# Performance work log

Hardware: AMD Instinct MI355X
Metric: run time of the kernel (lower is better)

Reference implementation:

```python
import jax, jax.numpy as jnp
import numpy as np

T, B = 512, 64
D = [2048, 128]; P = [512, 128]; H = [256, 128]
A, S, OUT = 128, 128, 256
SC = 0.05


def setup_inputs() -> dict:
    key = jax.random.key(0)
    ks = iter(jax.random.split(key, 64))
    def n(shape, sc=SC):
        return jax.random.normal(next(ks), shape, dtype=jnp.float32) * sc
    inp = {
        "x0": n((T, B, D[0]), 1.0),
        "x1": n((T, B, D[1]), 1.0),
        "s": n((B, S), 1.0),
    }
    for m in range(2):
        k = str(m)
        C = 2 * H[m]
        inp["emb_w" + k] = n((D[m], P[m])); inp["emb_b" + k] = n((P[m],))
        inp["fx_w" + k] = n((P[m], 4 * H[m])); inp["fx_b" + k] = n((4 * H[m],))
        inp["fh_w" + k] = n((H[m], 4 * H[m]))
        inp["bx_w" + k] = n((P[m], 4 * H[m])); inp["bx_b" + k] = n((4 * H[m],))
        inp["bh_w" + k] = n((H[m], 4 * H[m]))
        inp["atV_w" + k] = n((C, A)); inp["atV_b" + k] = n((A,))
        inp["atW_w" + k] = n((S, A)); inp["atW_b" + k] = n((A,))
        inp["atw_w" + k] = n((A, 1)); inp["atw_b" + k] = n((1,))
        inp["lgd_w" + k] = n((C, OUT)); inp["lgd_b" + k] = n((OUT,))
    return inp


def _lstm_scan(xg, Wh, reverse=False):
    # xg: [T,B,4H] precomputed input projections; Wh: [H,4H]
    Tn, Bn, H4 = xg.shape
    Hn = H4 // 4
    def step(carry, xt):
        c, h = carry
        g = xt + h @ Wh
        a, i, f, o = jnp.split(g, 4, axis=-1)  # chunk order as in torch.split
        c = jnp.tanh(a) * jax.nn.sigmoid(i) + c * jax.nn.sigmoid(f)
        h = jnp.tanh(c) * jax.nn.sigmoid(o)
        return (c, h), h
    init = (jnp.zeros((Bn, Hn), xg.dtype), jnp.zeros((Bn, Hn), xg.dtype))
    _, hs = jax.lax.scan(step, init, xg, reverse=reverse)
    return hs  # [T,B,H]


def _encode_mod(x, emb_w, emb_b, fx_w, fx_b, fh_w, bx_w, bx_b, bh_w):
    h0 = x @ emb_w + emb_b                       # [T,B,P]
    hf = _lstm_scan(h0 @ fx_w + fx_b, fh_w)      # forward LSTM
    hb = _lstm_scan(h0 @ bx_w + bx_b, bh_w, reverse=True)  # backward LSTM
    return jnp.concatenate([hf, hb], axis=-1)    # [T,B,2H]


def _attend(h, s, atV_w, atV_b, atW_w, atW_b, atw_w, atw_b):
    vh = h @ atV_w + atV_b                       # [T,B,A]
    ws = s @ atW_w + atW_b                       # [B,A]
    logits = (jnp.tanh(vh + ws) @ atw_w)[..., 0] + atw_b[0]  # [T,B]
    a = jax.nn.softmax(logits, axis=0)           # exp / sum over time (stable)
    return (a[..., None] * h).mean(0)            # [B,2H]; original uses mean over T


def _forward(x0, x1, s,
             emb_w0, emb_b0, fx_w0, fx_b0, fh_w0, bx_w0, bx_b0, bh_w0,
             atV_w0, atV_b0, atW_w0, atW_b0, atw_w0, atw_b0, lgd_w0, lgd_b0,
             emb_w1, emb_b1, fx_w1, fx_b1, fh_w1, bx_w1, bx_b1, bh_w1,
             atV_w1, atV_b1, atW_w1, atW_b1, atw_w1, atw_b1, lgd_w1, lgd_b1):
    h0 = _encode_mod(x0, emb_w0, emb_b0, fx_w0, fx_b0, fh_w0, bx_w0, bx_b0, bh_w0)
    h1 = _encode_mod(x1, emb_w1, emb_b1, fx_w1, fx_b1, fh_w1, bx_w1, bx_b1, bh_w1)
    c0 = _attend(h0, s, atV_w0, atV_b0, atW_w0, atW_b0, atw_w0, atw_b0)
    c1 = _attend(h1, s, atV_w1, atV_b1, atW_w1, atW_b1, atw_w1, atw_b1)
    g = (c0 @ lgd_w0 + lgd_b0) + (c1 @ lgd_w1 + lgd_b1)  # simple modality fusion
    return jnp.tanh(g)  # [B,OUT]


def reference(x0, x1, s,
              emb_w0, emb_b0, fx_w0, fx_b0, fh_w0, bx_w0, bx_b0, bh_w0,
              atV_w0, atV_b0, atW_w0, atW_b0, atw_w0, atw_b0, lgd_w0, lgd_b0,
              emb_w1, emb_b1, fx_w1, fx_b1, fh_w1, bx_w1, bx_b1, bh_w1,
              atV_w1, atV_b1, atW_w1, atW_b1, atw_w1, atw_b1, lgd_w1, lgd_b1):
    return _forward(x0, x1, s,
                    emb_w0, emb_b0, fx_w0, fx_b0, fh_w0, bx_w0, bx_b0, bh_w0,
                    atV_w0, atV_b0, atW_w0, atW_b0, atw_w0, atw_b0, lgd_w0, lgd_b0,
                    emb_w1, emb_b1, fx_w1, fx_b1, fh_w1, bx_w1, bx_b1, bh_w1,
                    atV_w1, atV_b1, atW_w1, atW_b1, atw_w1, atw_b1, lgd_w1, lgd_b1)
```

## Files before the change

### kernel.cpp

```cpp
#include <hip/hip_runtime.h>

typedef __attribute__((ext_vector_type(4))) float  f32x4;
typedef __attribute__((ext_vector_type(8))) short  short8;
typedef __attribute__((ext_vector_type(4))) short  short4v;
typedef __attribute__((ext_vector_type(4))) int    int4v;

__device__ __forceinline__ float bf2f(short s){
  unsigned u = ((unsigned)(unsigned short)s) << 16;
  float f; __builtin_memcpy(&f, &u, 4); return f;
}
__device__ __forceinline__ short f2bf(float x){
  unsigned u; __builtin_memcpy(&u, &x, 4);
  u = (u + 0x7fffu + ((u >> 16) & 1u)) >> 16;
  return (short)u;
}
__device__ __forceinline__ float sigm(float x){ return 1.f / (1.f + __expf(-x)); }
__device__ __forceinline__ float ftanh(float x){ return 1.f - 2.f / (__expf(2.f * x) + 1.f); }

__device__ __forceinline__ short8 ld_b128_sc1(const short* p){
  short8 r;
  asm volatile("global_load_dwordx4 %0, %1, off sc1" : "=&v"(r) : "v"(p) : "memory");
  return r;
}
__device__ __forceinline__ int4v ld_i4_sc1(const int* p){
  int4v r;
  asm volatile("global_load_dwordx4 %0, %1, off sc1" : "=&v"(r) : "v"(p) : "memory");
  return r;
}
__device__ __forceinline__ void st_dword_sc1(int* p, int v){
  asm volatile("global_store_dword %0, %1, off sc1" :: "v"(p), "v"(v) : "memory");
}
__device__ __forceinline__ void wait_vm0(){
  asm volatile("s_waitcnt vmcnt(0)" ::: "memory");
  __builtin_amdgcn_sched_barrier(0);
}

__global__ __launch_bounds__(256) void transpose_cvt(const float* __restrict__ W,
                                                     short* __restrict__ Wt,
                                                     int K, int N)
{
  __shared__ float tile[32][33];
  int kt = blockIdx.x * 32, nt = blockIdx.y * 32;
  int tx = threadIdx.x & 31, ty = threadIdx.x >> 5;
#pragma unroll
  for (int i = 0; i < 4; i++) {
    int k = kt + ty + i * 8, n = nt + tx;
    if (k < K && n < N) tile[ty + i * 8][tx] = W[(size_t)k * N + n];
  }
  __syncthreads();
#pragma unroll
  for (int i = 0; i < 4; i++) {
    int n = nt + ty + i * 8, k = kt + tx;
    if (n < N && k < K) Wt[(size_t)n * K + k] = f2bf(tile[tx][ty + i * 8]);
  }
}

template<int AF32, int OF32>
__global__ __launch_bounds__(256) void gemm_bias(const void* __restrict__ Av,
                                                 const short* __restrict__ Bt,
                                                 const float* __restrict__ bias,
                                                 void* __restrict__ Cv,
                                                 int M, int N, int K)
{
  __shared__ __align__(16) short As[128 * 40];
  __shared__ __align__(16) short Bs[128 * 40];
  int tid  = threadIdx.x;
  int col0 = blockIdx.x * 128, row0 = blockIdx.y * 128;
  int lane = tid & 63, wave = tid >> 6;
  int wm = (wave >> 1) * 64, wn = (wave & 1) * 64;

  f32x4 acc[4][4];
  for (int mi = 0; mi < 4; mi++)
    for (int ni = 0; ni < 4; ni++)
      for (int q = 0; q < 4; q++) acc[mi][ni][q] = 0.f;

  for (int kt = 0; kt < K; kt += 32) {
    __syncthreads();
    if (AF32) {
      const float* A = (const float*)Av;
      for (int i = 0; i < 4; i++) {
        int idx = tid + i * 256;
        int r = idx >> 3, c4 = (idx & 7) << 2;
        f32x4 v = *(const f32x4*)(A + (size_t)(row0 + r) * K + kt + c4);
        short4v o;
        for (int q = 0; q < 4; q++) o[q] = f2bf(v[q]);
        *(short4v*)&As[r * 40 + c4] = o;
      }
    } else {
      const short* A = (const short*)Av;
      for (int i = 0; i < 2; i++) {
        int idx = tid + i * 256;
        int r = idx >> 2, c8 = (idx & 3) << 3;
        short8 v = *(const short8*)(A + (size_t)(row0 + r) * K + kt + c8);
        *(short8*)&As[r * 40 + c8] = v;
      }
    }
    for (int i = 0; i < 2; i++) {
      int idx = tid + i * 256;
      int r = idx >> 2, c8 = (idx & 3) << 3;
      short8 v = *(const short8*)(Bt + (size_t)(col0 + r) * K + kt + c8);
      *(short8*)&Bs[r * 40 + c8] = v;
    }
    __syncthreads();

    int fr = lane & 15, fo = (lane >> 4) << 3;
    short8 af[4], bfr[4];
    for (int mi = 0; mi < 4; mi++) af[mi]  = *(short8*)&As[(wm + mi * 16 + fr) * 40 + fo];
    for (int ni = 0; ni < 4; ni++) bfr[ni] = *(short8*)&Bs[(wn + ni * 16 + fr) * 40 + fo];
    for (int mi = 0; mi < 4; mi++)
      for (int ni = 0; ni < 4; ni++)
        acc[mi][ni] = __builtin_amdgcn_mfma_f32_16x16x32_bf16(af[mi], bfr[ni], acc[mi][ni], 0, 0, 0);
  }

  int efr = lane & 15, efrow = (lane >> 4) << 2;
  for (int ni = 0; ni < 4; ni++) {
    int col = col0 + wn + ni * 16 + efr;
    float bv = bias[col];
    for (int mi = 0; mi < 4; mi++) {
      for (int q = 0; q < 4; q++) {
        int row = row0 + wm + mi * 16 + efrow + q;
        float v = acc[mi][ni][q] + bv;
        if (OF32) ((float*)Cv)[(size_t)row * N + col] = v;
        else      ((short*)Cv)[(size_t)row * N + col] = f2bf(v);
      }
    }
  }
}

__global__ __launch_bounds__(128) void att_ws_kernel(const float* __restrict__ s,
                                                     const float* __restrict__ atW,
                                                     const float* __restrict__ atWb,
                                                     float* __restrict__ ws)
{
  int b = blockIdx.x, a = threadIdx.x;
  float acc = atWb[a];
  for (int k = 0; k < 128; k++) acc += s[b * 128 + k] * atW[k * 128 + a];
  ws[b * 128 + a] = acc;
}

template<int H, int NB>
__device__ __forceinline__ void persistent_scan(
    const short* __restrict__ xg, const float* __restrict__ Wh,
    short* __restrict__ hall, int* __restrict__ flags,
    int wg, int dir, float* gl)
{
  constexpr int C = 2 * H, H4 = 4 * H, KB = H / 32;
  int tid = threadIdx.x, lane = tid & 63, w = tid >> 6;
  int j0 = wg * 8, dircol = dir ? H : 0;
  int n = lane & 15, ko = (lane >> 4) << 3;

  short8 bw[2][KB];
#pragma unroll
  for (int nt = 0; nt < 2; nt++) {
    int col = (n >> 2) * H + j0 + nt * 4 + (n & 3);
#pragma unroll
    for (int kb = 0; kb < KB; kb++)
#pragma unroll
      for (int e = 0; e < 8; e++)
        bw[nt][kb][e] = f2bf(Wh[(size_t)(kb * 32 + ko + e) * H4 + col]);
  }

  int batch0 = w * 16 + ((lane >> 4) << 2);
  int rowA   = w * 16 + n;
  int eb = tid >> 2, ejp = tid & 3;
  float c0 = 0.f, c1 = 0.f;

  int t = dir ? 511 : 0;
  short xgr[2][4];
#pragma unroll
  for (int nt = 0; nt < 2; nt++) {
    int col = (n >> 2) * H + j0 + nt * 4 + (n & 3);
#pragma unroll
    for (int q = 0; q < 4; q++)
      xgr[nt][q] = xg[(size_t)(t * 64 + batch0 + q) * H4 + col];
  }

  for (int s = 0; s < 512; s++) {
    t = dir ? 511 - s : s;
    f32x4 acc[2];
#pragma unroll
    for (int q = 0; q < 4; q++) { acc[0][q] = 0.f; acc[1][q] = 0.f; }

    if (s > 0) {
      int tprev = dir ? t + 1 : t - 1;
      const short* hb = hall + ((size_t)tprev * 64 + rowA) * C + dircol;
      short8 hv[KB];
#pragma unroll
      for (int kb = 0; kb < KB; kb++)
        hv[kb] = ld_b128_sc1(hb + kb * 32 + ko);
      wait_vm0();
#pragma unroll
      for (int kb = 0; kb < KB; kb++) {
        acc[0] = __builtin_amdgcn_mfma_f32_16x16x32_bf16(hv[kb], bw[0][kb], acc[0], 0, 0, 0);
        acc[1] = __builtin_amdgcn_mfma_f32_16x16x32_bf16(hv[kb], bw[1][kb], acc[1], 0, 0, 0);
      }
    }

#pragma unroll
    for (int nt = 0; nt < 2; nt++) {
      int gcol = (n >> 2) * 8 + nt * 4 + (n & 3);
#pragma unroll
      for (int q = 0; q < 4; q++)
        gl[(batch0 + q) * 33 + gcol] = acc[nt][q] + bf2f(xgr[nt][q]);
    }
    __syncthreads();

    {
      const float* gb = gl + eb * 33 + ejp * 2;
      float a0 = gb[0],  a1 = gb[1];
      float i0 = gb[8],  i1 = gb[9];
      float f0 = gb[16], f1 = gb[17];
      float o0 = gb[24], o1 = gb[25];
      c0 = ftanh(a0) * sigm(i0) + c0 * sigm(f0);
      c1 = ftanh(a1) * sigm(i1) + c1 * sigm(f1);
      unsigned h0 = (unsigned short)f2bf(ftanh(c0) * sigm(o0));
      unsigned h1 = (unsigned short)f2bf(ftanh(c1) * sigm(o1));
      st_dword_sc1((int*)(hall + ((size_t)t * 64 + eb) * C + dircol + j0 + ejp * 2),
                   (int)(h0 | (h1 << 16)));
    }

    if (s < 511) {
      wait_vm0();
      __syncthreads();
      if (tid == 0) st_dword_sc1(flags + wg, s + 1);

      int tn = dir ? t - 1 : t + 1;
#pragma unroll
      for (int nt = 0; nt < 2; nt++) {
        int col = (n >> 2) * H + j0 + nt * 4 + (n & 3);
#pragma unroll
        for (int q = 0; q < 4; q++)
          xgr[nt][q] = xg[(size_t)(tn * 64 + batch0 + q) * H4 + col];
      }

      if (tid == 0) {
        for (;;) {
          int4v f[NB / 4];
#pragma unroll
          for (int i = 0; i < NB / 4; i++) f[i] = ld_i4_sc1(flags + i * 4);
          wait_vm0();
          int ok = 1;
#pragma unroll
          for (int i = 0; i < NB / 4; i++)
#pragma unroll
            for (int j = 0; j < 4; j++) ok &= (f[i][j] > s);
          if (ok) break;
          __builtin_amdgcn_s_sleep(1);
        }
      }
      __syncthreads();
    }
  }
}

__global__ __launch_bounds__(256) void lstm_persistent(
    const short* __restrict__ xgf0, const short* __restrict__ xgb0,
    const short* __restrict__ xgf1, const short* __restrict__ xgb1,
    const float* __restrict__ fh0, const float* __restrict__ bh0,
    const float* __restrict__ fh1, const float* __restrict__ bh1,
    short* __restrict__ hall0, short* __restrict__ hall1, int* __restrict__ bar)
{
  __shared__ float gl[64 * 33];
  int bx = blockIdx.x;
  if (bx < 64) {
    int dir = bx >> 5, wg = bx & 31;
    persistent_scan<256, 32>(dir ? xgb0 : xgf0, dir ? bh0 : fh0, hall0,
                             bar + (dir ? 64 : 0), wg, dir, gl);
  } else {
    int r = bx - 64, dir = r >> 4, wg = r & 15;
    persistent_scan<128, 16>(dir ? xgb1 : xgf1, dir ? bh1 : fh1, hall1,
                             bar + 128 + (dir ? 64 : 0), wg, dir, gl);
  }
}

__global__ __launch_bounds__(256) void logits_kernel(const float* __restrict__ vh,
                                                     const float* __restrict__ ws,
                                                     const float* __restrict__ atw,
                                                     const float* __restrict__ atwb,
                                                     float* __restrict__ lg)
{
  int wid  = (int)((blockIdx.x * 256 + threadIdx.x) >> 6);
  int lane = threadIdx.x & 63;
  if (wid >= 32768) return;
  int b = wid & 63;
  float x0 = vh[(size_t)wid * 128 + lane]      + ws[b * 128 + lane];
  float x1 = vh[(size_t)wid * 128 + 64 + lane] + ws[b * 128 + 64 + lane];
  float v = ftanh(x0) * atw[lane] + ftanh(x1) * atw[64 + lane];
  for (int off = 32; off; off >>= 1) v += __shfl_down(v, off);
  if (lane == 0) lg[wid] = v + atwb[0];
}

__global__ __launch_bounds__(256) void softmax_ctx(const float* __restrict__ lg,
                                                   const short* __restrict__ hall,
                                                   float* __restrict__ ctx, int C)
{
  int b = blockIdx.x, tid = threadIdx.x, lane = tid & 63, wv = tid >> 6;
  __shared__ float ebuf[512];
  __shared__ float red[8];
  float l0 = lg[tid * 64 + b];
  float l1 = lg[(tid + 256) * 64 + b];
  float m = fmaxf(l0, l1);
  for (int o = 32; o; o >>= 1) m = fmaxf(m, __shfl_xor(m, o));
  if (lane == 0) red[wv] = m;
  __syncthreads();
  m = fmaxf(fmaxf(red[0], red[1]), fmaxf(red[2], red[3]));
  float e0 = __expf(l0 - m), e1 = __expf(l1 - m);
  ebuf[tid] = e0; ebuf[tid + 256] = e1;
  float sm = e0 + e1;
  for (int o = 32; o; o >>= 1) sm += __shfl_xor(sm, o);
  if (lane == 0) red[4 + wv] = sm;
  __syncthreads();
  sm = red[4] + red[5] + red[6] + red[7];
  float inv = 1.f / (sm * 512.f);
  for (int c = tid; c < C; c += 256) {
    float acc = 0.f;
    const short* hp = hall + (size_t)b * C + c;
    for (int t = 0; t < 512; t++) acc += ebuf[t] * bf2f(hp[(size_t)t * 64 * C]);
    ctx[b * C + c] = acc * inv;
  }
}

__global__ __launch_bounds__(256) void final_kernel(const float* __restrict__ ctx0,
                                                    const float* __restrict__ ctx1,
                                                    const float* __restrict__ w0,
                                                    const float* __restrict__ b0,
                                                    const float* __restrict__ w1,
                                                    const float* __restrict__ b1,
                                                    float* __restrict__ out)
{
  int b = blockIdx.x, o = threadIdx.x;
  float acc = b0[o] + b1[o];
  for (int c = 0; c < 512; c++) acc += ctx0[b * 512 + c] * w0[c * 256 + o];
  for (int c = 0; c < 256; c++) acc += ctx1[b * 256 + c] * w1[c * 256 + o];
  out[b * 256 + o] = ftanh(acc);
}

extern "C" void kernel_launch(void* const* d_in, const int* in_sizes, int n_in,
                              void* d_out, int out_size, void* d_ws, size_t ws_size,
                              hipStream_t stream)
{
  const float* x0    = (const float*)d_in[0];
  const float* x1    = (const float*)d_in[1];
  const float* sIn   = (const float*)d_in[2];
  const float* emb_w0 = (const float*)d_in[3];  const float* emb_b0 = (const float*)d_in[4];
  const float* fx_w0  = (const float*)d_in[5];  const float* fx_b0  = (const float*)d_in[6];
  const float* fh_w0  = (const float*)d_in[7];
  const float* bx_w0  = (const float*)d_in[8];  const float* bx_b0  = (const float*)d_in[9];
  const float* bh_w0  = (const float*)d_in[10];
  const float* atV_w0 = (const float*)d_in[11]; const float* atV_b0 = (const float*)d_in[12];
  const float* atW_w0 = (const float*)d_in[13]; const float* atW_b0 = (const float*)d_in[14];
  const float* atw_w0 = (const float*)d_in[15]; const float* atw_b0 = (const float*)d_in[16];
  const float* lgd_w0 = (const float*)d_in[17]; const float* lgd_b0 = (const float*)d_in[18];
  const float* emb_w1 = (const float*)d_in[19]; const float* emb_b1 = (const float*)d_in[20];
  const float* fx_w1  = (const float*)d_in[21]; const float* fx_b1  = (const float*)d_in[22];
  const float* fh_w1  = (const float*)d_in[23];
  const float* bx_w1  = (const float*)d_in[24]; const float* bx_b1  = (const float*)d_in[25];
  const float* bh_w1  = (const float*)d_in[26];
  const float* atV_w1 = (const float*)d_in[27]; const float* atV_b1 = (const float*)d_in[28];
  const float* atW_w1 = (const float*)d_in[29]; const float* atW_b1 = (const float*)d_in[30];
  const float* atw_w1 = (const float*)d_in[31]; const float* atw_b1 = (const float*)d_in[32];
  const float* lgd_w1 = (const float*)d_in[33]; const float* lgd_b1 = (const float*)d_in[34];
  float* out = (float*)d_out;

  char* wp = (char*)d_ws;
  auto alloc = [&](size_t bytes) -> void* {
    void* p = wp; wp += (bytes + 255) & ~(size_t)255; return p;
  };
  int*   bar   = (int*)alloc(1024);
  short* h0_0  = (short*)alloc(32768ull * 512 * 2);
  short* h0_1  = (short*)alloc(32768ull * 128 * 2);
  short* xgf0  = (short*)alloc(32768ull * 1024 * 2);
  short* xgb0  = (short*)alloc(32768ull * 1024 * 2);
  short* xgf1  = (short*)alloc(32768ull * 512 * 2);
  short* xgb1  = (short*)alloc(32768ull * 512 * 2);
  short* hall0 = (short*)alloc(32768ull * 512 * 2);
  short* hall1 = (short*)alloc(32768ull * 256 * 2);
  float* vh0   = (float*)alloc(32768ull * 128 * 4);
  float* vh1   = (float*)alloc(32768ull * 128 * 4);
  float* wsb0  = (float*)alloc(64 * 128 * 4);
  float* wsb1  = (float*)alloc(64 * 128 * 4);
  float* lg0   = (float*)alloc(32768 * 4);
  float* lg1   = (float*)alloc(32768 * 4);
  float* ctx0  = (float*)alloc(64 * 512 * 4);
  float* ctx1  = (float*)alloc(64 * 256 * 4);
  short* emb_w0t = (short*)alloc(512ull  * 2048 * 2);
  short* fx_w0t  = (short*)alloc(1024ull * 512 * 2);
  short* bx_w0t  = (short*)alloc(1024ull * 512 * 2);
  short* emb_w1t = (short*)alloc(128ull  * 128 * 2);
  short* fx_w1t  = (short*)alloc(512ull  * 128 * 2);
  short* bx_w1t  = (short*)alloc(512ull  * 128 * 2);
  short* atV_w0t = (short*)alloc(128ull  * 512 * 2);
  short* atV_w1t = (short*)alloc(128ull  * 256 * 2);

  transpose_cvt<<<dim3(64, 16), 256, 0, stream>>>(emb_w0, emb_w0t, 2048, 512);
  transpose_cvt<<<dim3(16, 32), 256, 0, stream>>>(fx_w0,  fx_w0t,  512, 1024);
  transpose_cvt<<<dim3(16, 32), 256, 0, stream>>>(bx_w0,  bx_w0t,  512, 1024);
  transpose_cvt<<<dim3(4, 4),   256, 0, stream>>>(emb_w1, emb_w1t, 128, 128);
  transpose_cvt<<<dim3(4, 16),  256, 0, stream>>>(fx_w1,  fx_w1t,  128, 512);
  transpose_cvt<<<dim3(4, 16),  256, 0, stream>>>(bx_w1,  bx_w1t,  128, 512);
  transpose_cvt<<<dim3(16, 4),  256, 0, stream>>>(atV_w0, atV_w0t, 512, 128);
  transpose_cvt<<<dim3(8, 4),   256, 0, stream>>>(atV_w1, atV_w1t, 256, 128);

  gemm_bias<1, 0><<<dim3(4, 256), 256, 0, stream>>>(x0, emb_w0t, emb_b0, h0_0, 32768, 512, 2048);
  gemm_bias<1, 0><<<dim3(1, 256), 256, 0, stream>>>(x1, emb_w1t, emb_b1, h0_1, 32768, 128, 128);
  gemm_bias<0, 0><<<dim3(8, 256), 256, 0, stream>>>(h0_0, fx_w0t, fx_b0, xgf0, 32768, 1024, 512);
  gemm_bias<0, 0><<<dim3(8, 256), 256, 0, stream>>>(h0_0, bx_w0t, bx_b0, xgb0, 32768, 1024, 512);
  gemm_bias<0, 0><<<dim3(4, 256), 256, 0, stream>>>(h0_1, fx_w1t, fx_b1, xgf1, 32768, 512, 128);
  gemm_bias<0, 0><<<dim3(4, 256), 256, 0, stream>>>(h0_1, bx_w1t, bx_b1, xgb1, 32768, 512, 128);
  att_ws_kernel<<<64, 128, 0, stream>>>(sIn, atW_w0, atW_b0, wsb0);
  att_ws_kernel<<<64, 128, 0, stream>>>(sIn, atW_w1, atW_b1, wsb1);

  hipMemsetAsync(bar, 0, 1024, stream);
  lstm_persistent<<<96, 256, 0, stream>>>(xgf0, xgb0, xgf1, xgb1,
                                          fh_w0, bh_w0, fh_w1, bh_w1,
                                          hall0, hall1, bar);

  gemm_bias<0, 1><<<dim3(1, 256), 256, 0, stream>>>(hall0, atV_w0t, atV_b0, vh0, 32768, 128, 512);
  gemm_bias<0, 1><<<dim3(1, 256), 256, 0, stream>>>(hall1, atV_w1t, atV_b1, vh1, 32768, 128, 256);
  logits_kernel<<<8192, 256, 0, stream>>>(vh0, wsb0, atw_w0, atw_b0, lg0);
  logits_kernel<<<8192, 256, 0, stream>>>(vh1, wsb1, atw_w1, atw_b1, lg1);
  softmax_ctx<<<64, 256, 0, stream>>>(lg0, hall0, ctx0, 512);
  softmax_ctx<<<64, 256, 0, stream>>>(lg1, hall1, ctx1, 256);
  final_kernel<<<64, 256, 0, stream>>>(ctx0, ctx1, lgd_w0, lgd_b0, lgd_w1, lgd_b1, out);
}
```

Before: 2.410 ms.

## Use direct global-to-LDS loads in GEMM, pre-convert inputs, batch weight transposes

The GEMM now stages A and B tiles with global_load_lds 16-byte direct loads into unpadded LDS, which removes the register round trip. To make this possible, the fp32 inputs x0 and x1 are first converted to bf16 by a separate kernel into scratch buffers that reuse the xgf buffers. The eight weight transpose launches are merged into one kernel driven by a descriptor table. The trade-offs are an extra full pass over x0 for the conversion and LDS bank conflicts from dropping the row padding.

```diff
diff --git a/kernel.cpp b/kernel.cpp
--- a/kernel.cpp
+++ b/kernel.cpp
@@ -35,39 +35,69 @@
   __builtin_amdgcn_sched_barrier(0);
 }
 
-__global__ __launch_bounds__(256) void transpose_cvt(const float* __restrict__ W,
-                                                     short* __restrict__ Wt,
-                                                     int K, int N)
+__device__ __forceinline__ void gload16(const short* g, short* l){
+  __builtin_amdgcn_global_load_lds(
+      (const __attribute__((address_space(1))) void*)g,
+      (__attribute__((address_space(3))) void*)l, 16, 0, 0);
+}
+
+__global__ __launch_bounds__(256) void cvt_f32_bf16(const float* __restrict__ in,
+                                                    short* __restrict__ out, long n)
+{
+  long i = ((long)blockIdx.x * 256 + threadIdx.x) * 4;
+  long stride = (long)gridDim.x * 1024;
+  for (; i < n; i += stride) {
+    f32x4 v = *(const f32x4*)(in + i);
+    short4v o;
+#pragma unroll
+    for (int q = 0; q < 4; q++) o[q] = f2bf(v[q]);
+    *(short4v*)(out + i) = o;
+  }
+}
+
+struct TD { const float* W; short* Wt; int K, N, b0, nb, nbx; };
+struct TD8 { TD d[8]; };
+
+__global__ __launch_bounds__(256) void transpose_all(TD8 ds)
 {
   __shared__ float tile[32][33];
-  int kt = blockIdx.x * 32, nt = blockIdx.y * 32;
-  int tx = threadIdx.x & 31, ty = threadIdx.x >> 5;
-#pragma unroll
-  for (int i = 0; i < 4; i++) {
-    int k = kt + ty + i * 8, n = nt + tx;
-    if (k < K && n < N) tile[ty + i * 8][tx] = W[(size_t)k * N + n];
-  }
-  __syncthreads();
-#pragma unroll
-  for (int i = 0; i < 4; i++) {
-    int n = nt + ty + i * 8, k = kt + tx;
-    if (n < N && k < K) Wt[(size_t)n * K + k] = f2bf(tile[tx][ty + i * 8]);
-  }
-}
-
-template<int AF32, int OF32>
-__global__ __launch_bounds__(256) void gemm_bias(const void* __restrict__ Av,
-                                                 const short* __restrict__ Bt,
-                                                 const float* __restrict__ bias,
-                                                 void* __restrict__ Cv,
-                                                 int M, int N, int K)
-{
-  __shared__ __align__(16) short As[128 * 40];
-  __shared__ __align__(16) short Bs[128 * 40];
+  int bx = blockIdx.x;
+#pragma unroll
+  for (int m = 0; m < 8; m++) {
+    TD d = ds.d[m];
+    if (bx >= d.b0 && bx < d.b0 + d.nb) {
+      int lb = bx - d.b0;
+      int kt = (lb % d.nbx) * 32, nt = (lb / d.nbx) * 32;
+      int tx = threadIdx.x & 31, ty = threadIdx.x >> 5;
+#pragma unroll
+      for (int i = 0; i < 4; i++) {
+        int k = kt + ty + i * 8, n = nt + tx;
+        if (k < d.K && n < d.N) tile[ty + i * 8][tx] = d.W[(size_t)k * d.N + n];
+      }
+      __syncthreads();
+#pragma unroll
+      for (int i = 0; i < 4; i++) {
+        int n = nt + ty + i * 8, k = kt + tx;
+        if (n < d.N && k < d.K) d.Wt[(size_t)n * d.K + k] = f2bf(tile[tx][ty + i * 8]);
+      }
+      return;
+    }
+  }
+}
+
+__global__ __launch_bounds__(256) void gemm_bt(const short* __restrict__ A,
+                                               const short* __restrict__ Bt,
+                                               const float* __restrict__ bias,
+                                               void* __restrict__ Cv,
+                                               int M, int N, int K, int OF32)
+{
+  __shared__ __align__(16) short As[128 * 32];
+  __shared__ __align__(16) short Bs[128 * 32];
   int tid  = threadIdx.x;
   int col0 = blockIdx.x * 128, row0 = blockIdx.y * 128;
-  int lane = tid & 63, wave = tid >> 6;
-  int wm = (wave >> 1) * 64, wn = (wave & 1) * 64;
+  int lane = tid & 63, w = tid >> 6;
+  int wm = (w >> 1) * 64, wn = (w & 1) * 64;
+  int lr = lane >> 2, lc = (lane & 3) * 8;
 
   f32x4 acc[4][4];
   for (int mi = 0; mi < 4; mi++)
@@ -76,37 +106,18 @@
 
   for (int kt = 0; kt < K; kt += 32) {
     __syncthreads();
-    if (AF32) {
-      const float* A = (const float*)Av;
-      for (int i = 0; i < 4; i++) {
-        int idx = tid + i * 256;
-        int r = idx >> 3, c4 = (idx & 7) << 2;
-        f32x4 v = *(const f32x4*)(A + (size_t)(row0 + r) * K + kt + c4);
-        short4v o;
-        for (int q = 0; q < 4; q++) o[q] = f2bf(v[q]);
-        *(short4v*)&As[r * 40 + c4] = o;
-      }
-    } else {
-      const short* A = (const short*)Av;
-      for (int i = 0; i < 2; i++) {
-        int idx = tid + i * 256;
-        int r = idx >> 2, c8 = (idx & 3) << 3;
-        short8 v = *(const short8*)(A + (size_t)(row0 + r) * K + kt + c8);
-        *(short8*)&As[r * 40 + c8] = v;
-      }
-    }
+#pragma unroll
     for (int i = 0; i < 2; i++) {
-      int idx = tid + i * 256;
-      int r = idx >> 2, c8 = (idx & 3) << 3;
-      short8 v = *(const short8*)(Bt + (size_t)(col0 + r) * K + kt + c8);
-      *(short8*)&Bs[r * 40 + c8] = v;
+      int rbase = w * 32 + i * 16;
+      gload16(A  + (size_t)(row0 + rbase + lr) * K + kt + lc, &As[rbase * 32]);
+      gload16(Bt + (size_t)(col0 + rbase + lr) * K + kt + lc, &Bs[rbase * 32]);
     }
     __syncthreads();
 
     int fr = lane & 15, fo = (lane >> 4) << 3;
     short8 af[4], bfr[4];
-    for (int mi = 0; mi < 4; mi++) af[mi]  = *(short8*)&As[(wm + mi * 16 + fr) * 40 + fo];
-    for (int ni = 0; ni < 4; ni++) bfr[ni] = *(short8*)&Bs[(wn + ni * 16 + fr) * 40 + fo];
+    for (int mi = 0; mi < 4; mi++) af[mi]  = *(short8*)&As[(wm + mi * 16 + fr) * 32 + fo];
+    for (int ni = 0; ni < 4; ni++) bfr[ni] = *(short8*)&Bs[(wn + ni * 16 + fr) * 32 + fo];
     for (int mi = 0; mi < 4; mi++)
       for (int ni = 0; ni < 4; ni++)
         acc[mi][ni] = __builtin_amdgcn_mfma_f32_16x16x32_bf16(af[mi], bfr[ni], acc[mi][ni], 0, 0, 0);
@@ -391,22 +402,36 @@
   short* bx_w1t  = (short*)alloc(512ull  * 128 * 2);
   short* atV_w0t = (short*)alloc(128ull  * 512 * 2);
   short* atV_w1t = (short*)alloc(128ull  * 256 * 2);
-
-  transpose_cvt<<<dim3(64, 16), 256, 0, stream>>>(emb_w0, emb_w0t, 2048, 512);
-  transpose_cvt<<<dim3(16, 32), 256, 0, stream>>>(fx_w0,  fx_w0t,  512, 1024);
-  transpose_cvt<<<dim3(16, 32), 256, 0, stream>>>(bx_w0,  bx_w0t,  512, 1024);
-  transpose_cvt<<<dim3(4, 4),   256, 0, stream>>>(emb_w1, emb_w1t, 128, 128);
-  transpose_cvt<<<dim3(4, 16),  256, 0, stream>>>(fx_w1,  fx_w1t,  128, 512);
-  transpose_cvt<<<dim3(4, 16),  256, 0, stream>>>(bx_w1,  bx_w1t,  128, 512);
-  transpose_cvt<<<dim3(16, 4),  256, 0, stream>>>(atV_w0, atV_w0t, 512, 128);
-  transpose_cvt<<<dim3(8, 4),   256, 0, stream>>>(atV_w1, atV_w1t, 256, 128);
-
-  gemm_bias<1, 0><<<dim3(4, 256), 256, 0, stream>>>(x0, emb_w0t, emb_b0, h0_0, 32768, 512, 2048);
-  gemm_bias<1, 0><<<dim3(1, 256), 256, 0, stream>>>(x1, emb_w1t, emb_b1, h0_1, 32768, 128, 128);
-  gemm_bias<0, 0><<<dim3(8, 256), 256, 0, stream>>>(h0_0, fx_w0t, fx_b0, xgf0, 32768, 1024, 512);
-  gemm_bias<0, 0><<<dim3(8, 256), 256, 0, stream>>>(h0_0, bx_w0t, bx_b0, xgb0, 32768, 1024, 512);
-  gemm_bias<0, 0><<<dim3(4, 256), 256, 0, stream>>>(h0_1, fx_w1t, fx_b1, xgf1, 32768, 512, 128);
-  gemm_bias<0, 0><<<dim3(4, 256), 256, 0, stream>>>(h0_1, bx_w1t, bx_b1, xgb1, 32768, 512, 128);
+  short* x0b = xgf0;
+  short* x1b = xgf1;
+
+  cvt_f32_bf16<<<2048, 256, 0, stream>>>(x0, x0b, 32768ll * 2048);
+  cvt_f32_bf16<<<512,  256, 0, stream>>>(x1, x1b, 32768ll * 128);
+
+  {
+    TD8 ds; int b0 = 0;
+    auto set = [&](int i, const float* W, short* Wt, int K, int N){
+      int nbx = (K + 31) / 32, nby = (N + 31) / 32;
+      ds.d[i] = TD{W, Wt, K, N, b0, nbx * nby, nbx};
+      b0 += nbx * nby;
+    };
+    set(0, emb_w0, emb_w0t, 2048, 512);
+    set(1, fx_w0,  fx_w0t,  512, 1024);
+    set(2, bx_w0,  bx_w0t,  512, 1024);
+    set(3, emb_w1, emb_w1t, 128, 128);
+    set(4, fx_w1,  fx_w1t,  128, 512);
+    set(5, bx_w1,  bx_w1t,  128, 512);
+    set(6, atV_w0, atV_w0t, 512, 128);
+    set(7, atV_w1, atV_w1t, 256, 128);
+    transpose_all<<<b0, 256, 0, stream>>>(ds);
+  }
+
+  gemm_bt<<<dim3(4, 256), 256, 0, stream>>>(x0b, emb_w0t, emb_b0, h0_0, 32768, 512, 2048, 0);
+  gemm_bt<<<dim3(1, 256), 256, 0, stream>>>(x1b, emb_w1t, emb_b1, h0_1, 32768, 128, 128, 0);
+  gemm_bt<<<dim3(8, 256), 256, 0, stream>>>(h0_0, fx_w0t, fx_b0, xgf0, 32768, 1024, 512, 0);
+  gemm_bt<<<dim3(8, 256), 256, 0, stream>>>(h0_0, bx_w0t, bx_b0, xgb0, 32768, 1024, 512, 0);
+  gemm_bt<<<dim3(4, 256), 256, 0, stream>>>(h0_1, fx_w1t, fx_b1, xgf1, 32768, 512, 128, 0);
+  gemm_bt<<<dim3(4, 256), 256, 0, stream>>>(h0_1, bx_w1t, bx_b1, xgb1, 32768, 512, 128, 0);
   att_ws_kernel<<<64, 128, 0, stream>>>(sIn, atW_w0, atW_b0, wsb0);
   att_ws_kernel<<<64, 128, 0, stream>>>(sIn, atW_w1, atW_b1, wsb1);
 
@@ -415,8 +440,8 @@
                                           fh_w0, bh_w0, fh_w1, bh_w1,
                                           hall0, hall1, bar);
 
-  gemm_bias<0, 1><<<dim3(1, 256), 256, 0, stream>>>(hall0, atV_w0t, atV_b0, vh0, 32768, 128, 512);
-  gemm_bias<0, 1><<<dim3(1, 256), 256, 0, stream>>>(hall1, atV_w1t, atV_b1, vh1, 32768, 128, 256);
+  gemm_bt<<<dim3(1, 256), 256, 0, stream>>>(hall0, atV_w0t, atV_b0, vh0, 32768, 128, 512, 1);
+  gemm_bt<<<dim3(1, 256), 256, 0, stream>>>(hall1, atV_w1t, atV_b1, vh1, 32768, 128, 256, 1);
   logits_kernel<<<8192, 256, 0, stream>>>(vh0, wsb0, atw_w0, atw_b0, lg0);
   logits_kernel<<<8192, 256, 0, stream>>>(vh1, wsb1, atw_w1, atw_b1, lg1);
   softmax_ctx<<<64, 256, 0, stream>>>(lg0, hall0, ctx0, 512);
```

New measurement: 2.395 ms. No clear change (-0.7%).
